# Performance work log

Measured on AMD Instinct MI355X. Metric: run time of the kernel, lower is better.

## Reference

```python
import jax, jax.numpy as jnp
import numpy as np
from jax import lax

B, C_IN, T = 256, 1, 1632
HID, CB_DIM, NUM_TOK, NUM_Q = 64, 512, 1024, 2


def conv_k2s2(x, W, b):
    # Conv1d(kernel=2, stride=2): x [B,Ci,T] -> [B,Co,T//2]; W [Co,Ci,2]
    Bx, Ci, Tx = x.shape
    xr = x.reshape(Bx, Ci, Tx // 2, 2)
    return jnp.einsum('bitk,oik->bot', xr, W) + b[None, :, None]


def convT_k2s2(x, W, b):
    # ConvTranspose1d(kernel=2, stride=2): x [B,Ci,T] -> [B,Co,2T]; W [Ci,Co,2] (torch layout)
    Bx, Ci, Tx = x.shape
    y = jnp.einsum('bit,iok->botk', x, W)  # [B,Co,T,2]
    Co = W.shape[1]
    return y.reshape(Bx, Co, 2 * Tx) + b[None, :, None]


def conv1x1(x, W, b):
    # W [Co,Ci]
    return jnp.einsum('bit,oi->bot', x, W) + b[None, :, None]


def residual_vq(x, codebooks):
    # x [B,t,D]; codebooks [NUM_Q, NUM_TOK, D]. Euclidean argmin + straight-through.
    residual = x
    quantized_out = jnp.zeros_like(x)
    all_idx, all_loss = [], []
    for q in range(codebooks.shape[0]):
        cb = codebooks[q]  # [N,D]
        # squared euclidean distance, single large GEMM
        d2 = (jnp.sum(residual ** 2, -1, keepdims=True)
              - 2.0 * jnp.einsum('btd,nd->btn', residual, cb)
              + jnp.sum(cb ** 2, -1))  # [B,t,N]
        idx = jnp.argmin(d2, axis=-1)  # [B,t]
        quant = cb[idx]  # gather [B,t,D]
        # commitment loss (codebook treated as fixed / EMA-updated)
        loss = jnp.mean((lax.stop_gradient(quant) - residual) ** 2)
        # straight-through estimator
        quant_st = residual + lax.stop_gradient(quant - residual)
        residual = residual - lax.stop_gradient(quant)
        quantized_out = quantized_out + quant_st
        all_idx.append(idx)
        all_loss.append(loss)
    return quantized_out, jnp.stack(all_idx, -1), jnp.stack(all_loss)


def setup_inputs() -> dict:
    key = jax.random.key(0)
    ks = jax.random.split(key, 16)
    s = 0.02
    return {
        'img': jax.random.normal(ks[0], (B, C_IN, T), jnp.float32),
        'W_e1': jax.random.normal(ks[1], (HID, C_IN, 2), jnp.float32) * s,
        'b_e1': jnp.zeros((HID,), jnp.float32),
        'W_e2': jax.random.normal(ks[2], (HID, HID, 2), jnp.float32) * s,
        'b_e2': jnp.zeros((HID,), jnp.float32),
        'W_e3': jax.random.normal(ks[3], (CB_DIM, HID), jnp.float32) * s,
        'b_e3': jnp.zeros((CB_DIM,), jnp.float32),
        'codebooks': jax.random.normal(ks[4], (NUM_Q, NUM_TOK, CB_DIM), jnp.float32),
        'Wt_d1': jax.random.normal(ks[5], (CB_DIM, HID, 2), jnp.float32) * s,
        'b_d1': jnp.zeros((HID,), jnp.float32),
        'Wt_d2': jax.random.normal(ks[6], (HID, HID, 2), jnp.float32) * s,
        'b_d2': jnp.zeros((HID,), jnp.float32),
        'W_d3': jax.random.normal(ks[7], (C_IN, HID), jnp.float32) * s,
        'b_d3': jnp.zeros((C_IN,), jnp.float32),
    }


def reference(img, W_e1, b_e1, W_e2, b_e2, W_e3, b_e3, codebooks,
              Wt_d1, b_d1, Wt_d2, b_d2, W_d3, b_d3):
    # encoder
    h = jax.nn.relu(conv_k2s2(img, W_e1, b_e1))
    h = jax.nn.relu(conv_k2s2(h, W_e2, b_e2))
    encoded = conv1x1(h, W_e3, b_e3)  # [B,512,408]
    # residual VQ over tokens
    x = jnp.transpose(encoded, (0, 2, 1))  # b c t -> b t c
    quantized, indices, commit_loss = residual_vq(x, codebooks)
    quantized = jnp.transpose(quantized, (0, 2, 1))  # b t c -> b c t
    # decoder
    d = jax.nn.relu(convT_k2s2(quantized, Wt_d1, b_d1))
    d = jax.nn.relu(convT_k2s2(d, Wt_d2, b_d2))
    out = conv1x1(d, W_d3, b_d3)  # [B,1,1632]
    recon_loss = jnp.mean((img - out) ** 2)
    return out, recon_loss, commit_loss, indices, quantized
```

## Files before the change

### kernel.cpp

```cpp
#include <hip/hip_runtime.h>

#define NB    256
#define TLEN  1632
#define HIDC  64
#define CBD   512
#define NTOK  1024
#define T2L   816
#define T4L   408
#define MTOK  (NB*T4L)
#define M2TOK (NB*T2L)
#define MOUT  (NB*TLEN)

#define DO_OUT    ((size_t)0)
#define DO_RECON  ((size_t)417792)
#define DO_IDX    ((size_t)417795)
#define DO_QUANT  ((size_t)626691)

typedef unsigned short u16;
typedef unsigned long long u64;
typedef __attribute__((ext_vector_type(8))) short short8;
typedef __attribute__((ext_vector_type(4))) float f32x4;
typedef __attribute__((ext_vector_type(8))) _Float16 half8;
typedef __attribute__((ext_vector_type(4))) _Float16 half4;

static constexpr size_t OFF_XR  = 0;
static constexpr size_t OFF_H1  = OFF_XR + (size_t)MTOK*512;
static constexpr size_t OFF_H2  = OFF_H1 + (size_t)NB*T2L*64;
static constexpr size_t OFF_BE2 = OFF_H2 + (size_t)NB*T4L*64;
static constexpr size_t OFF_BD1 = OFF_BE2 + 8192;
static constexpr size_t OFF_BD2 = OFF_BD1 + 65536;
static constexpr size_t OFF_BX1 = OFF_BD2 + 8192;
static constexpr size_t OFF_BX2 = OFF_BX1 + 128;
static constexpr size_t OFF_ZB  = OFF_BX2 + 128;
static constexpr size_t OFF_C2  = OFF_ZB + 128;
static constexpr size_t OFF_SLOT= OFF_C2 + 2048;
static constexpr size_t OFF_IDXI= OFF_SLOT + 1536;
static constexpr size_t OFF_KEYS= OFF_IDXI + (size_t)MTOK*2;
static constexpr size_t OFF_FC  = OFF_KEYS + (size_t)MTOK*4;
static constexpr size_t OFF_FLAG= OFF_FC + 4;
static constexpr size_t OFF_CBH = OFF_FLAG + (size_t)MTOK*2;
static constexpr size_t OFF_CBL = OFF_CBH + 524288;
static constexpr size_t OFF_P0  = OFF_CBL + 524288;
static constexpr size_t OFF_P1  = OFF_P0 + 131072;
static constexpr size_t OFF_PAIRS = OFF_P1 + 131072;

__device__ inline u64 shfl_xor_u64_w16(u64 v, int m) {
    unsigned lo = (unsigned)v, hi = (unsigned)(v >> 32);
    lo = __shfl_xor(lo, m, 16);
    hi = __shfl_xor(hi, m, 16);
    return (((u64)hi) << 32) | lo;
}
__device__ inline u64 packkey(float d, int n) {
    unsigned u = __float_as_uint(d);
    u = (u & 0x80000000u) ? ~u : (u | 0x80000000u);
    return (((u64)u) << 32) | (unsigned)n;
}
__device__ inline float unpackd(u64 k) {
    unsigned u = (unsigned)(k >> 32);
    u = (u & 0x80000000u) ? (u & 0x7fffffffu) : ~u;
    return __uint_as_float(u);
}
__device__ inline void merge2(u64& k1, u64& k2, u64 o1, u64 o2) {
    u64 n1 = (k1 < o1) ? k1 : o1;
    u64 hi = (k1 < o1) ? o1 : k1;
    u64 cand = (k1 <= o1) ? k2 : o2;
    u64 n2 = (hi < cand) ? hi : cand;
    k1 = n1; k2 = n2;
}
__device__ inline half4 cvt_h4(float4 v) {
    half4 h;
    h.x = (_Float16)v.x; h.y = (_Float16)v.y;
    h.z = (_Float16)v.z; h.w = (_Float16)v.w;
    return h;
}

__global__ void setup_kernel(const float* __restrict__ We2, const float* __restrict__ Wtd1,
                             const float* __restrict__ Wtd2, const float* __restrict__ bd1,
                             const float* __restrict__ bd2, const float* __restrict__ cbs,
                             float* __restrict__ Be2, float* __restrict__ Bd1,
                             float* __restrict__ Bd2, float* __restrict__ bx1, float* __restrict__ bx2,
                             u16* __restrict__ cbh, float* __restrict__ c2) {
    size_t t = (size_t)blockIdx.x * 256 + threadIdx.x;
    {
        float4 v = *(const float4*)(cbs + t * 4);
        *(half4*)&cbh[t * 4] = cvt_h4(v);
    }
    {
        int w = (int)(t >> 6);
        int lane = threadIdx.x & 63;
        if (w < 2048) {
            const float* r = cbs + (size_t)w * 512;
            float4 a = *(const float4*)(r + lane * 8);
            float4 b = *(const float4*)(r + lane * 8 + 4);
            float s = a.x*a.x + a.y*a.y + a.z*a.z + a.w*a.w + b.x*b.x + b.y*b.y + b.z*b.z + b.w*b.w;
            #pragma unroll
            for (int o = 32; o > 0; o >>= 1) s += __shfl_down(s, o, 64);
            if (lane == 0) c2[w] = s;
        }
    }
    size_t stride = (size_t)gridDim.x * 256;
    for (size_t x = t; x < 64 * 128; x += stride) {
        int c = (int)(x >> 7), k = (int)(x & 127);
        Be2[x] = We2[c * 128 + ((k & 63) << 1) + (k >> 6)];
    }
    for (size_t x = t; x < 128 * 512; x += stride) {
        int n = (int)(x >> 9), k = (int)(x & 511);
        Bd1[x] = Wtd1[k * 128 + n];
    }
    for (size_t x = t; x < 128 * 64; x += stride) {
        int n = (int)(x >> 6), k = (int)(x & 63);
        Bd2[x] = Wtd2[k * 128 + n];
    }
    for (size_t x = t; x < 128; x += stride) { bx1[x] = bd1[x >> 1]; bx2[x] = bd2[x >> 1]; }
}

__global__ void enc1_kernel(const float* __restrict__ img, const float* __restrict__ W,
                            const float* __restrict__ bias, float* __restrict__ h1) {
    int idx = blockIdx.x * 256 + threadIdx.x;
    int c = idx & 63;
    int t = (idx >> 6) % T2L;
    int b = idx / (64 * T2L);
    float v = W[c * 2] * img[(size_t)b * TLEN + 2 * t] +
              W[c * 2 + 1] * img[(size_t)b * TLEN + 2 * t + 1] + bias[c];
    h1[idx] = fmaxf(v, 0.f);
}

__global__ __launch_bounds__(256) void gemm_nt(const float* __restrict__ A, const float* __restrict__ Bw,
                        const float* __restrict__ bias, float* __restrict__ C,
                        int M, int N, int K, int amode, int relu) {
    __shared__ float As[32][132];
    __shared__ float Bs[32][68];
    int m0 = blockIdx.x * 128;
    int n0 = blockIdx.y * 64;
    int tid = threadIdx.x;
    int tx = tid & 15;
    int ty = tid >> 4;
    float acc[8][4];
    #pragma unroll
    for (int i = 0; i < 8; ++i)
        #pragma unroll
        for (int j = 0; j < 4; ++j) acc[i][j] = 0.f;

    for (int k0 = 0; k0 < K; k0 += 32) {
        #pragma unroll
        for (int i = 0; i < 4; ++i) {
            int idx = tid + i * 256;
            int row = idx >> 3;
            int kq = idx & 7;
            int m = m0 + row;
            size_t base;
            if (amode == 0) base = (size_t)m * K;
            else            base = (size_t)(((m / T4L) * T2L + 2 * (m % T4L)) * 64);
            float4 v = *(const float4*)(A + base + k0 + kq * 4);
            int kk = kq * 4;
            As[kk + 0][row] = v.x; As[kk + 1][row] = v.y;
            As[kk + 2][row] = v.z; As[kk + 3][row] = v.w;
        }
        #pragma unroll
        for (int i = 0; i < 2; ++i) {
            int idx = tid + i * 256;
            int row = idx >> 3;
            int kq = idx & 7;
            float4 v = *(const float4*)(Bw + (size_t)(n0 + row) * K + k0 + kq * 4);
            int kk = kq * 4;
            Bs[kk + 0][row] = v.x; Bs[kk + 1][row] = v.y;
            Bs[kk + 2][row] = v.z; Bs[kk + 3][row] = v.w;
        }
        __syncthreads();
        #pragma unroll
        for (int kk = 0; kk < 32; ++kk) {
            float a[8], bf[4];
            float4 a0 = *(const float4*)&As[kk][ty * 8];
            float4 a1 = *(const float4*)&As[kk][ty * 8 + 4];
            a[0]=a0.x; a[1]=a0.y; a[2]=a0.z; a[3]=a0.w;
            a[4]=a1.x; a[5]=a1.y; a[6]=a1.z; a[7]=a1.w;
            float4 b0 = *(const float4*)&Bs[kk][tx * 4];
            bf[0]=b0.x; bf[1]=b0.y; bf[2]=b0.z; bf[3]=b0.w;
            #pragma unroll
            for (int i = 0; i < 8; ++i)
                #pragma unroll
                for (int j = 0; j < 4; ++j) acc[i][j] += a[i] * bf[j];
        }
        __syncthreads();
    }
    #pragma unroll
    for (int i = 0; i < 8; ++i) {
        int m = m0 + ty * 8 + i;
        float4 v;
        v.x = acc[i][0] + bias[n0 + tx * 4 + 0];
        v.y = acc[i][1] + bias[n0 + tx * 4 + 1];
        v.z = acc[i][2] + bias[n0 + tx * 4 + 2];
        v.w = acc[i][3] + bias[n0 + tx * 4 + 3];
        if (relu) { v.x=fmaxf(v.x,0.f); v.y=fmaxf(v.y,0.f); v.z=fmaxf(v.z,0.f); v.w=fmaxf(v.w,0.f); }
        *(float4*)(C + (size_t)m * N + n0 + tx * 4) = v;
    }
}

template<int Q1>
__global__ __launch_bounds__(256, 2) void vq_f16_db(
    const float* __restrict__ Ap, const u16* __restrict__ cbh,
    const float* __restrict__ c2, const u64* __restrict__ prevkeys,
    const float* __restrict__ cb0, u64* __restrict__ pairs)
{
    __shared__ __align__(16) u16 As[2][128 * 40];
    __shared__ __align__(16) u16 Bh[2][256 * 40];
    int tid = threadIdx.x;
    int n0 = blockIdx.x * 256, m0 = blockIdx.y * 128;
    int lane = tid & 63, wid = tid >> 6;
    int lm = lane & 15, quad = lane >> 4;
    int wm = wid >> 1, wn = wid & 1;

    f32x4 acc[4][8];
    #pragma unroll
    for (int i = 0; i < 4; ++i)
        #pragma unroll
        for (int j = 0; j < 8; ++j) acc[i][j] = (f32x4){0.f, 0.f, 0.f, 0.f};

    int ar[4], acq[4], br[4], bcc[4];
    size_t coff[4];
    #pragma unroll
    for (int i = 0; i < 4; ++i) {
        int idx = tid + i * 256;
        ar[i] = idx >> 3; acq[i] = idx & 7;
        br[i] = idx >> 2; bcc[i] = idx & 3;
        if (Q1) {
            int i0 = (int)(prevkeys[m0 + ar[i]] & 0xFFFFFFFFull);
            coff[i] = (size_t)i0 * 512;
        }
    }

#define VQ_LOAD(K0, AV, CV, BV)                                                     \
    _Pragma("unroll")                                                               \
    for (int i = 0; i < 4; ++i) {                                                   \
        AV[i] = *(const float4*)(Ap + (size_t)(m0 + ar[i]) * 512 + (K0) + acq[i]*4);\
        if (Q1) CV[i] = *(const float4*)(cb0 + coff[i] + (K0) + acq[i]*4);          \
        BV[i] = *(const short8*)(cbh + (size_t)(n0 + br[i]) * 512 + (K0) + bcc[i]*8); \
    }

#define VQ_WRITE(BUF, AV, CV, BV)                                                   \
    _Pragma("unroll")                                                               \
    for (int i = 0; i < 4; ++i) {                                                   \
        float4 v = AV[i];                                                           \
        if (Q1) { v.x -= CV[i].x; v.y -= CV[i].y; v.z -= CV[i].z; v.w -= CV[i].w; } \
        *(half4*)&As[BUF][ar[i] * 40 + acq[i] * 4] = cvt_h4(v);                     \
        *(short8*)&Bh[BUF][br[i] * 40 + bcc[i] * 8] = BV[i];                        \
    }

#define VQ_COMPUTE(BUF) {                                                           \
        half8 ah[4];                                                                \
        _Pragma("unroll")                                                           \
        for (int mt = 0; mt < 4; ++mt)                                              \
            ah[mt] = *(const half8*)&As[BUF][(wm*64 + mt*16 + lm) * 40 + quad * 8]; \
        _Pragma("unroll")                                                           \
        for (int nt = 0; nt < 8; ++nt) {                                            \
            half8 bh = *(const half8*)&Bh[BUF][(wn*128 + nt*16 + lm) * 40 + quad*8];\
            _Pragma("unroll")                                                       \
            for (int mt = 0; mt < 4; ++mt)                                          \
                acc[mt][nt] = __builtin_amdgcn_mfma_f32_16x16x32_f16(ah[mt], bh, acc[mt][nt], 0, 0, 0); \
        }                                                                           \
    }

    float4 avA[4], cvA[4], avB[4], cvB[4];
    short8 bvA[4], bvB[4];
    (void)cvA; (void)cvB;

    VQ_LOAD(0, avA, cvA, bvA);
    VQ_WRITE(0, avA, cvA, bvA);
    VQ_LOAD(32, avB, cvB, bvB);
    __syncthreads();

    for (int tp = 0; tp < 8; ++tp) {
        {
            VQ_WRITE(1, avB, cvB, bvB);
            if (tp < 7) { int K0 = (2 * tp + 2) * 32; VQ_LOAD(K0, avA, cvA, bvA); }
            VQ_COMPUTE(0);
            __syncthreads();
        }
        {
            if (tp < 7) { VQ_WRITE(0, avA, cvA, bvA); }
            if (tp < 7) { int K0 = (2 * tp + 3) * 32; VQ_LOAD(K0, avB, cvB, bvB); }
            VQ_COMPUTE(1);
            __syncthreads();
        }
    }
#undef VQ_LOAD
#undef VQ_WRITE
#undef VQ_COMPUTE

    float c2v[8];
    #pragma unroll
    for (int nt = 0; nt < 8; ++nt) c2v[nt] = c2[n0 + wn * 128 + nt * 16 + lm];

    u64* scr = (u64*)&As[0][0];
    #pragma unroll
    for (int mt = 0; mt < 4; ++mt) {
        #pragma unroll
        for (int rg = 0; rg < 4; ++rg) {
            int tl = wm * 64 + mt * 16 + quad * 4 + rg;
            u64 k1 = ~0ull, k2 = ~0ull;
            #pragma unroll
            for (int nt = 0; nt < 8; ++nt) {
                float d = c2v[nt] - 2.0f * acc[mt][nt][rg];
                u64 k = packkey(d, n0 + wn * 128 + nt * 16 + lm);
                if (k < k1) { k2 = k1; k1 = k; } else if (k < k2) { k2 = k; }
            }
            #pragma unroll
            for (int s = 1; s < 16; s <<= 1) {
                u64 o1 = shfl_xor_u64_w16(k1, s);
                u64 o2 = shfl_xor_u64_w16(k2, s);
                merge2(k1, k2, o1, o2);
            }
            if (lm == 0) { scr[wn * 256 + tl * 2] = k1; scr[wn * 256 + tl * 2 + 1] = k2; }
        }
    }
    __syncthreads();
    if (tid < 128) {
        u64 a1 = scr[tid * 2], a2 = scr[tid * 2 + 1];
        merge2(a1, a2, scr[256 + tid * 2], scr[256 + tid * 2 + 1]);
        size_t base = (size_t)(m0 + tid) * 8 + blockIdx.x * 2;
        pairs[base] = a1; pairs[base + 1] = a2;
    }
}

__global__ void vq_reduce(const u64* __restrict__ pairs, u64* __restrict__ keybuf,
                          int* __restrict__ fc, int* __restrict__ flaglist, float tau) {
    int m = blockIdx.x * 256 + threadIdx.x;
    const u64* p = pairs + (size_t)m * 8;
    u64 k1 = ~0ull, k2 = ~0ull;
    #pragma unroll
    for (int i = 0; i < 8; ++i) {
        u64 k = p[i];
        if (k < k1) { k2 = k1; k1 = k; } else if (k < k2) { k2 = k; }
    }
    keybuf[m] = k1;
    if (unpackd(k2) - unpackd(k1) < tau) {
        int pos = atomicAdd(fc, 1);
        flaglist[pos] = m;
    }
}

__global__ void vq_rescue(const float* __restrict__ xr, const float* __restrict__ cb,
                          const float* __restrict__ c2, const float* __restrict__ cb0,
                          const u64* __restrict__ prevkeys,
                          const int* __restrict__ fc, const int* __restrict__ flaglist,
                          u64* __restrict__ keybuf) {
    __shared__ u64 red[4];
    int cnt = *fc;
    int lane = threadIdx.x & 63, wid = threadIdx.x >> 6;
    for (int f = blockIdx.x; f < cnt; f += gridDim.x) {
        int m = flaglist[f];
        float4 rv0 = *(const float4*)(xr + (size_t)m * 512 + lane * 8);
        float4 rv1 = *(const float4*)(xr + (size_t)m * 512 + lane * 8 + 4);
        if (cb0) {
            size_t co = (size_t)(prevkeys[m] & 0xFFFFFFFFull) * 512;
            float4 c0 = *(const float4*)(cb0 + co + lane * 8);
            float4 c1 = *(const float4*)(cb0 + co + lane * 8 + 4);
            rv0.x -= c0.x; rv0.y -= c0.y; rv0.z -= c0.z; rv0.w -= c0.w;
            rv1.x -= c1.x; rv1.y -= c1.y; rv1.z -= c1.z; rv1.w -= c1.w;
        }
        u64 best = ~0ull;
        for (int c = wid * 256; c < wid * 256 + 256; ++c) {
            const float* cp = cb + (size_t)c * 512 + lane * 8;
            float4 c0 = *(const float4*)cp;
            float4 c1 = *(const float4*)(cp + 4);
            float p = rv0.x*c0.x + rv0.y*c0.y + rv0.z*c0.z + rv0.w*c0.w
                    + rv1.x*c1.x + rv1.y*c1.y + rv1.z*c1.z + rv1.w*c1.w;
            #pragma unroll
            for (int s = 1; s < 64; s <<= 1) p += __shfl_xor(p, s, 64);
            u64 k = packkey(c2[c] - 2.0f * p, c);
            if (k < best) best = k;
        }
        if (lane == 0) red[wid] = best;
        __syncthreads();
        if (threadIdx.x == 0) {
            u64 b = red[0];
            if (red[1] < b) b = red[1];
            if (red[2] < b) b = red[2];
            if (red[3] < b) b = red[3];
            keybuf[m] = b;
        }
        __syncthreads();
    }
}

__global__ void commit_idx_kernel(const float* __restrict__ xr,
                                  const float* __restrict__ cb0f, const float* __restrict__ cb1f,
                                  const u64* __restrict__ keys0, const u64* __restrict__ keys1,
                                  float* __restrict__ idx_f, int* __restrict__ idx_i,
                                  float* __restrict__ slots) {
    int tid = threadIdx.x;
    int lane = tid & 63;
    int m = blockIdx.x * 4 + (tid >> 6);
    unsigned i0 = (unsigned)(keys0[m] & 0xFFFFFFFFull);
    unsigned i1 = (unsigned)(keys1[m] & 0xFFFFFFFFull);
    const float* x = xr + (size_t)m * 512 + lane * 8;
    const float* c0 = cb0f + (size_t)i0 * 512 + lane * 8;
    const float* c1 = cb1f + (size_t)i1 * 512 + lane * 8;
    float4 x0 = *(const float4*)x, x1 = *(const float4*)(x + 4);
    float4 a0 = *(const float4*)c0, a1 = *(const float4*)(c0 + 4);
    float4 b0 = *(const float4*)c1, b1 = *(const float4*)(c1 + 4);
    x0.x -= a0.x; x0.y -= a0.y; x0.z -= a0.z; x0.w -= a0.w;
    x1.x -= a1.x; x1.y -= a1.y; x1.z -= a1.z; x1.w -= a1.w;
    float s1 = x0.x*x0.x + x0.y*x0.y + x0.z*x0.z + x0.w*x0.w
             + x1.x*x1.x + x1.y*x1.y + x1.z*x1.z + x1.w*x1.w;
    x0.x -= b0.x; x0.y -= b0.y; x0.z -= b0.z; x0.w -= b0.w;
    x1.x -= b1.x; x1.y -= b1.y; x1.z -= b1.z; x1.w -= b1.w;
    float s2 = x0.x*x0.x + x0.y*x0.y + x0.z*x0.z + x0.w*x0.w
             + x1.x*x1.x + x1.y*x1.y + x1.z*x1.z + x1.w*x1.w;
    #pragma unroll
    for (int o = 32; o > 0; o >>= 1) { s1 += __shfl_down(s1, o, 64); s2 += __shfl_down(s2, o, 64); }
    if (lane == 0) {
        atomicAdd(&slots[512 + (m & 511)], s1);
        atomicAdd(&slots[1024 + (m & 511)], s2);
        idx_f[(size_t)m * 2]     = (float)i0;
        idx_f[(size_t)m * 2 + 1] = (float)i1;
        idx_i[m * 2] = (int)i0;
        idx_i[m * 2 + 1] = (int)i1;
    }
}

__global__ void quant_out_kernel(const float* __restrict__ cb0, const float* __restrict__ cb1,
                                 const int* __restrict__ idxi, float* __restrict__ out4) {
    __shared__ float buf[64][129];
    __shared__ int i0s[64], i1s[64];
    int b = blockIdx.x;
    int t0 = blockIdx.y * 64;
    int c0 = blockIdx.z * 128;
    int tid = threadIdx.x;
    if (tid < 64) {
        int t = t0 + tid;
        int i0 = 0, i1 = 0;
        if (t < T4L) { i0 = idxi[(b * T4L + t) * 2]; i1 = idxi[(b * T4L + t) * 2 + 1]; }
        i0s[tid] = i0; i1s[tid] = i1;
    }
    __syncthreads();
    int cl = tid & 127, th = tid >> 7;
    for (int t = th; t < 64; t += 2) {
        if (t0 + t < T4L)
            buf[t][cl] = cb0[(size_t)i0s[t] * 512 + c0 + cl] + cb1[(size_t)i1s[t] * 512 + c0 + cl];
    }
    __syncthreads();
    int lane = tid & 63, ch = tid >> 6;
    for (int cc = ch; cc < 128; cc += 4) {
        int t = t0 + lane;
        if (t < T4L) out4[((size_t)b * 512 + c0 + cc) * T4L + t] = buf[lane][cc];
    }
}

__global__ void d1_gather_kernel(const float* __restrict__ P0, const float* __restrict__ P1,
                                 const int* __restrict__ idxi, const float* __restrict__ bx1,
                                 float* __restrict__ d1) {
    int x = blockIdx.x * 256 + threadIdx.x;
    int n = x & 127;
    int m = x >> 7;
    int b = m / T4L, t = m % T4L;
    int i0 = idxi[m * 2], i1 = idxi[m * 2 + 1];
    float v = P0[i0 * 128 + n] + P1[i1 * 128 + n] + bx1[n];
    v = fmaxf(v, 0.f);
    d1[((size_t)(b * T2L + 2 * t + (n & 1))) * 64 + (n >> 1)] = v;
}

__global__ __launch_bounds__(256) void dec2_fused(
    const float* __restrict__ d1, const float* __restrict__ Bd2, const float* __restrict__ bx2,
    const float* __restrict__ W3, const float* __restrict__ b3, const float* __restrict__ img,
    float* __restrict__ out, float* __restrict__ slots)
{
    __shared__ float As[32][132];
    __shared__ float Bs[32][132];
    __shared__ float w3s[64];
    int m0 = blockIdx.x * 128;
    int tid = threadIdx.x;
    int tx = tid & 15;
    int ty = tid >> 4;
    if (tid < 64) w3s[tid] = W3[tid];
    float acc[8][8];
    #pragma unroll
    for (int i = 0; i < 8; ++i)
        #pragma unroll
        for (int j = 0; j < 8; ++j) acc[i][j] = 0.f;

    for (int k0 = 0; k0 < 64; k0 += 32) {
        #pragma unroll
        for (int i = 0; i < 4; ++i) {
            int idx = tid + i * 256;
            int row = idx >> 3;
            int kq = idx & 7;
            float4 v = *(const float4*)(d1 + (size_t)(m0 + row) * 64 + k0 + kq * 4);
            int kk = kq * 4;
            As[kk + 0][row] = v.x; As[kk + 1][row] = v.y;
            As[kk + 2][row] = v.z; As[kk + 3][row] = v.w;
        }
        #pragma unroll
        for (int i = 0; i < 4; ++i) {
            int idx = tid + i * 256;
            int row = idx >> 3;
            int kq = idx & 7;
            float4 v = *(const float4*)(Bd2 + (size_t)row * 64 + k0 + kq * 4);
            int kk = kq * 4;
            Bs[kk + 0][row] = v.x; Bs[kk + 1][row] = v.y;
            Bs[kk + 2][row] = v.z; Bs[kk + 3][row] = v.w;
        }
        __syncthreads();
        #pragma unroll
        for (int kk = 0; kk < 32; ++kk) {
            float a[8], bf[8];
            float4 a0 = *(const float4*)&As[kk][ty * 8];
            float4 a1 = *(const float4*)&As[kk][ty * 8 + 4];
            a[0]=a0.x; a[1]=a0.y; a[2]=a0.z; a[3]=a0.w;
            a[4]=a1.x; a[5]=a1.y; a[6]=a1.z; a[7]=a1.w;
            float4 b0 = *(const float4*)&Bs[kk][tx * 4];
            float4 b1 = *(const float4*)&Bs[kk][64 + tx * 4];
            bf[0]=b0.x; bf[1]=b0.y; bf[2]=b0.z; bf[3]=b0.w;
            bf[4]=b1.x; bf[5]=b1.y; bf[6]=b1.z; bf[7]=b1.w;
            #pragma unroll
            for (int i = 0; i < 8; ++i)
                #pragma unroll
                for (int j = 0; j < 8; ++j) acc[i][j] += a[i] * bf[j];
        }
        __syncthreads();
    }
    float bb3 = b3[0];
    float local = 0.f;
    #pragma unroll
    for (int i = 0; i < 8; ++i) {
        float s0 = 0.f, s1 = 0.f;
        #pragma unroll
        for (int j = 0; j < 4; ++j) {
            int n = tx * 4 + j;
            float v = fmaxf(acc[i][j] + bx2[n], 0.f);
            float w = w3s[n >> 1];
            if (j & 1) s1 += w * v; else s0 += w * v;
            int n2 = 64 + tx * 4 + j;
            float v2 = fmaxf(acc[i][j + 4] + bx2[n2], 0.f);
            float w2 = w3s[n2 >> 1];
            if (j & 1) s1 += w2 * v2; else s0 += w2 * v2;
        }
        #pragma unroll
        for (int o = 8; o > 0; o >>= 1) { s0 += __shfl_down(s0, o, 16); s1 += __shfl_down(s1, o, 16); }
        if (tx == 0) {
            int m = m0 + ty * 8 + i;
            int b = m / T2L, t2 = m % T2L;
            size_t o0 = (size_t)b * TLEN + 2 * t2;
            float v0 = s0 + bb3, v1 = s1 + bb3;
            out[o0] = v0; out[o0 + 1] = v1;
            float e0 = img[o0] - v0, e1 = img[o0 + 1] - v1;
            local += e0 * e0 + e1 * e1;
        }
    }
    if (tx == 0) atomicAdd(&slots[(blockIdx.x * 16 + ty) & 511], local);
}

__global__ void finalize_kernel(const float* __restrict__ slots, float* __restrict__ out_scalars) {
    __shared__ float red[256];
    int tid = threadIdx.x;
    for (int which = 0; which < 3; ++which) {
        float s = slots[which * 512 + tid] + slots[which * 512 + tid + 256];
        red[tid] = s; __syncthreads();
        for (int st = 128; st > 0; st >>= 1) { if (tid < st) red[tid] += red[tid + st]; __syncthreads(); }
        if (tid == 0) {
            float denom = (which == 0) ? (float)MOUT : (float)((size_t)MTOK * 512);
            out_scalars[which] = red[0] / denom;
        }
        __syncthreads();
    }
}

extern "C" void kernel_launch(void* const* d_in, const int* in_sizes, int n_in,
                              void* d_out, int out_size, void* d_ws, size_t ws_size,
                              hipStream_t stream) {
    const float* img  = (const float*)d_in[0];
    const float* We1  = (const float*)d_in[1];
    const float* be1  = (const float*)d_in[2];
    const float* We2  = (const float*)d_in[3];
    const float* be2  = (const float*)d_in[4];
    const float* We3  = (const float*)d_in[5];
    const float* be3  = (const float*)d_in[6];
    const float* cbs  = (const float*)d_in[7];
    const float* Wtd1 = (const float*)d_in[8];
    const float* bd1  = (const float*)d_in[9];
    const float* Wtd2 = (const float*)d_in[10];
    const float* bd2  = (const float*)d_in[11];
    const float* Wd3  = (const float*)d_in[12];
    const float* bd3  = (const float*)d_in[13];

    float* w = (float*)d_ws;
    float* xr   = w + OFF_XR;
    float* h1   = w + OFF_H1;
    float* h2   = w + OFF_H2;
    float* Be2  = w + OFF_BE2;
    float* Bd1  = w + OFF_BD1;
    float* Bd2  = w + OFF_BD2;
    float* bx1  = w + OFF_BX1;
    float* bx2  = w + OFF_BX2;
    float* zerob= w + OFF_ZB;
    float* c2   = w + OFF_C2;
    float* slots= w + OFF_SLOT;
    int*   idxi = (int*)(w + OFF_IDXI);
    u64*   keys = (u64*)(w + OFF_KEYS);
    int*   fc   = (int*)(w + OFF_FC);
    int*   flag = (int*)(w + OFF_FLAG);
    u16*   cbh  = (u16*)(w + OFF_CBH);
    float* P0   = w + OFF_P0;
    float* P1   = w + OFF_P1;
    u64*   pairs= (u64*)(w + OFF_PAIRS);

    float* outp = (float*)d_out;
    float* out0   = outp + DO_OUT;
    float* oscal  = outp + DO_RECON;
    float* idxf   = outp + DO_IDX;
    float* qout   = outp + DO_QUANT;

    hipMemsetAsync(slots, 0, 1536 * sizeof(float), stream);
    hipMemsetAsync(fc, 0, 2 * sizeof(int), stream);
    hipMemsetAsync(zerob, 0, 128 * sizeof(float), stream);

    setup_kernel<<<1024, 256, 0, stream>>>(We2, Wtd1, Wtd2, bd1, bd2, cbs,
                                           Be2, Bd1, Bd2, bx1, bx2, cbh, c2);

    const float* cb1p = cbs + (size_t)NTOK * CBD;

    gemm_nt<<<dim3(8, 2), 256, 0, stream>>>(cbs,  Bd1, zerob, P0, 1024, 128, 512, 0, 0);
    gemm_nt<<<dim3(8, 2), 256, 0, stream>>>(cb1p, Bd1, zerob, P1, 1024, 128, 512, 0, 0);

    enc1_kernel<<<(NB * T2L * HIDC) / 256, 256, 0, stream>>>(img, We1, be1, h1);
    gemm_nt<<<dim3(MTOK / 128, 1), 256, 0, stream>>>(h1, Be2, be2, h2, MTOK, 64, 128, 1, 1);
    gemm_nt<<<dim3(MTOK / 128, 8), 256, 0, stream>>>(h2, We3, be3, xr, MTOK, 512, 64, 0, 0);

    vq_f16_db<0><<<dim3(4, MTOK / 128), 256, 0, stream>>>(xr, cbh, c2, nullptr, nullptr, pairs);
    vq_reduce<<<MTOK / 256, 256, 0, stream>>>(pairs, keys, fc + 0, flag, 0.05f);
    vq_rescue<<<1024, 256, 0, stream>>>(xr, cbs, c2, nullptr, nullptr, fc + 0, flag, keys);
    vq_f16_db<1><<<dim3(4, MTOK / 128), 256, 0, stream>>>(xr, cbh + (size_t)NTOK * 512,
                                                          c2 + NTOK, keys, cbs, pairs);
    vq_reduce<<<MTOK / 256, 256, 0, stream>>>(pairs, keys + MTOK, fc + 1, flag + MTOK, 0.15f);
    vq_rescue<<<1024, 256, 0, stream>>>(xr, cb1p, c2 + NTOK, cbs, keys, fc + 1, flag + MTOK, keys + MTOK);

    commit_idx_kernel<<<MTOK / 4, 256, 0, stream>>>(xr, cbs, cb1p, keys, keys + MTOK, idxf, idxi, slots);

    quant_out_kernel<<<dim3(NB, 7, 4), 256, 0, stream>>>(cbs, cb1p, idxi, qout);

    d1_gather_kernel<<<(MTOK * 128) / 256, 256, 0, stream>>>(P0, P1, idxi, bx1, h1);
    dec2_fused<<<M2TOK / 128, 256, 0, stream>>>(h1, Bd2, bx2, Wd3, bd3, img, out0, slots);

    finalize_kernel<<<1, 256, 0, stream>>>(slots, oscal);
}
```

Before: 1.176 ms.

## Shrink VQ distance GEMM tile to 128x128 and subtract residual in fp16

The VQ distance GEMM tile drops from 128x256 to 128x128, which halves the accumulator registers and shared memory per block. Occupancy is raised to 3 blocks per CU, and the codebook dimension now uses 8 blocks instead of 4. The second-stage residual now subtracts the fp16 copy of the previous codeword instead of the fp32 one, which halves that gather traffic but adds extra rounding error before the argmin. Candidate pairs per token double to 16, and the pairs buffer now reuses the h2 scratch region, so each A tile is loaded twice as often.

```diff
diff --git a/kernel.cpp b/kernel.cpp
--- a/kernel.cpp
+++ b/kernel.cpp
@@ -42,7 +42,6 @@
 static constexpr size_t OFF_CBL = OFF_CBH + 524288;
 static constexpr size_t OFF_P0  = OFF_CBL + 524288;
 static constexpr size_t OFF_P1  = OFF_P0 + 131072;
-static constexpr size_t OFF_PAIRS = OFF_P1 + 131072;
 
 __device__ inline u64 shfl_xor_u64_w16(u64 v, int m) {
     unsigned lo = (unsigned)v, hi = (unsigned)(v >> 32);
@@ -71,6 +70,14 @@
     half4 h;
     h.x = (_Float16)v.x; h.y = (_Float16)v.y;
     h.z = (_Float16)v.z; h.w = (_Float16)v.w;
+    return h;
+}
+__device__ inline half8 cvt_h8(float4 v0, float4 v1) {
+    half8 h;
+    h[0] = (_Float16)v0.x; h[1] = (_Float16)v0.y;
+    h[2] = (_Float16)v0.z; h[3] = (_Float16)v0.w;
+    h[4] = (_Float16)v1.x; h[5] = (_Float16)v1.y;
+    h[6] = (_Float16)v1.z; h[7] = (_Float16)v1.w;
     return h;
 }
 
@@ -197,88 +204,89 @@
 }
 
 template<int Q1>
-__global__ __launch_bounds__(256, 2) void vq_f16_db(
+__global__ __launch_bounds__(256, 3) void vq_f16_db(
     const float* __restrict__ Ap, const u16* __restrict__ cbh,
     const float* __restrict__ c2, const u64* __restrict__ prevkeys,
-    const float* __restrict__ cb0, u64* __restrict__ pairs)
+    const u16* __restrict__ cb0h, u64* __restrict__ pairs)
 {
     __shared__ __align__(16) u16 As[2][128 * 40];
-    __shared__ __align__(16) u16 Bh[2][256 * 40];
+    __shared__ __align__(16) u16 Bs[2][128 * 40];
     int tid = threadIdx.x;
-    int n0 = blockIdx.x * 256, m0 = blockIdx.y * 128;
+    int n0 = blockIdx.x * 128, m0 = blockIdx.y * 128;
     int lane = tid & 63, wid = tid >> 6;
     int lm = lane & 15, quad = lane >> 4;
     int wm = wid >> 1, wn = wid & 1;
 
-    f32x4 acc[4][8];
+    f32x4 acc[4][4];
     #pragma unroll
     for (int i = 0; i < 4; ++i)
         #pragma unroll
-        for (int j = 0; j < 8; ++j) acc[i][j] = (f32x4){0.f, 0.f, 0.f, 0.f};
-
-    int ar[4], acq[4], br[4], bcc[4];
-    size_t coff[4];
-    #pragma unroll
-    for (int i = 0; i < 4; ++i) {
+        for (int j = 0; j < 4; ++j) acc[i][j] = (f32x4){0.f, 0.f, 0.f, 0.f};
+
+    int rw[2], cq[2];
+    size_t coff[2];
+    #pragma unroll
+    for (int i = 0; i < 2; ++i) {
         int idx = tid + i * 256;
-        ar[i] = idx >> 3; acq[i] = idx & 7;
-        br[i] = idx >> 2; bcc[i] = idx & 3;
+        rw[i] = idx >> 2; cq[i] = idx & 3;
         if (Q1) {
-            int i0 = (int)(prevkeys[m0 + ar[i]] & 0xFFFFFFFFull);
+            int i0 = (int)(prevkeys[m0 + rw[i]] & 0xFFFFFFFFull);
             coff[i] = (size_t)i0 * 512;
         }
     }
 
-#define VQ_LOAD(K0, AV, CV, BV)                                                     \
-    _Pragma("unroll")                                                               \
-    for (int i = 0; i < 4; ++i) {                                                   \
-        AV[i] = *(const float4*)(Ap + (size_t)(m0 + ar[i]) * 512 + (K0) + acq[i]*4);\
-        if (Q1) CV[i] = *(const float4*)(cb0 + coff[i] + (K0) + acq[i]*4);          \
-        BV[i] = *(const short8*)(cbh + (size_t)(n0 + br[i]) * 512 + (K0) + bcc[i]*8); \
-    }
-
-#define VQ_WRITE(BUF, AV, CV, BV)                                                   \
-    _Pragma("unroll")                                                               \
-    for (int i = 0; i < 4; ++i) {                                                   \
-        float4 v = AV[i];                                                           \
-        if (Q1) { v.x -= CV[i].x; v.y -= CV[i].y; v.z -= CV[i].z; v.w -= CV[i].w; } \
-        *(half4*)&As[BUF][ar[i] * 40 + acq[i] * 4] = cvt_h4(v);                     \
-        *(short8*)&Bh[BUF][br[i] * 40 + bcc[i] * 8] = BV[i];                        \
-    }
-
-#define VQ_COMPUTE(BUF) {                                                           \
-        half8 ah[4];                                                                \
-        _Pragma("unroll")                                                           \
-        for (int mt = 0; mt < 4; ++mt)                                              \
-            ah[mt] = *(const half8*)&As[BUF][(wm*64 + mt*16 + lm) * 40 + quad * 8]; \
-        _Pragma("unroll")                                                           \
-        for (int nt = 0; nt < 8; ++nt) {                                            \
-            half8 bh = *(const half8*)&Bh[BUF][(wn*128 + nt*16 + lm) * 40 + quad*8];\
-            _Pragma("unroll")                                                       \
-            for (int mt = 0; mt < 4; ++mt)                                          \
+#define VQ_LOAD(K0, AV0, AV1, CH, BV)                                                 \
+    _Pragma("unroll")                                                                 \
+    for (int i = 0; i < 2; ++i) {                                                     \
+        AV0[i] = *(const float4*)(Ap + (size_t)(m0 + rw[i]) * 512 + (K0) + cq[i]*8);  \
+        AV1[i] = *(const float4*)(Ap + (size_t)(m0 + rw[i]) * 512 + (K0) + cq[i]*8 + 4);\
+        if (Q1) CH[i] = *(const half8*)(cb0h + coff[i] + (K0) + cq[i]*8);             \
+        BV[i] = *(const short8*)(cbh + (size_t)(n0 + rw[i]) * 512 + (K0) + cq[i]*8);  \
+    }
+
+#define VQ_WRITE(BUF, AV0, AV1, CH, BV)                                               \
+    _Pragma("unroll")                                                                 \
+    for (int i = 0; i < 2; ++i) {                                                     \
+        half8 hv = cvt_h8(AV0[i], AV1[i]);                                            \
+        if (Q1) hv = hv - CH[i];                                                      \
+        *(half8*)&As[BUF][rw[i] * 40 + cq[i] * 8] = hv;                               \
+        *(short8*)&Bs[BUF][rw[i] * 40 + cq[i] * 8] = BV[i];                           \
+    }
+
+#define VQ_COMPUTE(BUF) {                                                             \
+        half8 ah[4];                                                                  \
+        _Pragma("unroll")                                                             \
+        for (int mt = 0; mt < 4; ++mt)                                                \
+            ah[mt] = *(const half8*)&As[BUF][(wm*64 + mt*16 + lm) * 40 + quad * 8];   \
+        _Pragma("unroll")                                                             \
+        for (int nt = 0; nt < 4; ++nt) {                                              \
+            half8 bh = *(const half8*)&Bs[BUF][(wn*64 + nt*16 + lm) * 40 + quad * 8]; \
+            _Pragma("unroll")                                                         \
+            for (int mt = 0; mt < 4; ++mt)                                            \
                 acc[mt][nt] = __builtin_amdgcn_mfma_f32_16x16x32_f16(ah[mt], bh, acc[mt][nt], 0, 0, 0); \
-        }                                                                           \
-    }
-
-    float4 avA[4], cvA[4], avB[4], cvB[4];
-    short8 bvA[4], bvB[4];
-    (void)cvA; (void)cvB;
-
-    VQ_LOAD(0, avA, cvA, bvA);
-    VQ_WRITE(0, avA, cvA, bvA);
-    VQ_LOAD(32, avB, cvB, bvB);
+        }                                                                             \
+    }
+
+    float4 a0A[2], a1A[2], a0B[2], a1B[2];
+    half8 chA[2], chB[2];
+    short8 bvA[2], bvB[2];
+    (void)chA; (void)chB;
+
+    VQ_LOAD(0, a0A, a1A, chA, bvA);
+    VQ_WRITE(0, a0A, a1A, chA, bvA);
+    VQ_LOAD(32, a0B, a1B, chB, bvB);
     __syncthreads();
 
     for (int tp = 0; tp < 8; ++tp) {
         {
-            VQ_WRITE(1, avB, cvB, bvB);
-            if (tp < 7) { int K0 = (2 * tp + 2) * 32; VQ_LOAD(K0, avA, cvA, bvA); }
+            VQ_WRITE(1, a0B, a1B, chB, bvB);
+            if (tp < 7) { int K0 = (2 * tp + 2) * 32; VQ_LOAD(K0, a0A, a1A, chA, bvA); }
             VQ_COMPUTE(0);
             __syncthreads();
         }
         {
-            if (tp < 7) { VQ_WRITE(0, avA, cvA, bvA); }
-            if (tp < 7) { int K0 = (2 * tp + 3) * 32; VQ_LOAD(K0, avB, cvB, bvB); }
+            if (tp < 7) { VQ_WRITE(0, a0A, a1A, chA, bvA); }
+            if (tp < 7) { int K0 = (2 * tp + 3) * 32; VQ_LOAD(K0, a0B, a1B, chB, bvB); }
             VQ_COMPUTE(1);
             __syncthreads();
         }
@@ -287,9 +295,9 @@
 #undef VQ_WRITE
 #undef VQ_COMPUTE
 
-    float c2v[8];
-    #pragma unroll
-    for (int nt = 0; nt < 8; ++nt) c2v[nt] = c2[n0 + wn * 128 + nt * 16 + lm];
+    float c2v[4];
+    #pragma unroll
+    for (int nt = 0; nt < 4; ++nt) c2v[nt] = c2[n0 + wn * 64 + nt * 16 + lm];
 
     u64* scr = (u64*)&As[0][0];
     #pragma unroll
@@ -299,9 +307,9 @@
             int tl = wm * 64 + mt * 16 + quad * 4 + rg;
             u64 k1 = ~0ull, k2 = ~0ull;
             #pragma unroll
-            for (int nt = 0; nt < 8; ++nt) {
+            for (int nt = 0; nt < 4; ++nt) {
                 float d = c2v[nt] - 2.0f * acc[mt][nt][rg];
-                u64 k = packkey(d, n0 + wn * 128 + nt * 16 + lm);
+                u64 k = packkey(d, n0 + wn * 64 + nt * 16 + lm);
                 if (k < k1) { k2 = k1; k1 = k; } else if (k < k2) { k2 = k; }
             }
             #pragma unroll
@@ -317,7 +325,7 @@
     if (tid < 128) {
         u64 a1 = scr[tid * 2], a2 = scr[tid * 2 + 1];
         merge2(a1, a2, scr[256 + tid * 2], scr[256 + tid * 2 + 1]);
-        size_t base = (size_t)(m0 + tid) * 8 + blockIdx.x * 2;
+        size_t base = (size_t)(m0 + tid) * 16 + blockIdx.x * 2;
         pairs[base] = a1; pairs[base + 1] = a2;
     }
 }
@@ -325,10 +333,10 @@
 __global__ void vq_reduce(const u64* __restrict__ pairs, u64* __restrict__ keybuf,
                           int* __restrict__ fc, int* __restrict__ flaglist, float tau) {
     int m = blockIdx.x * 256 + threadIdx.x;
-    const u64* p = pairs + (size_t)m * 8;
+    const u64* p = pairs + (size_t)m * 16;
     u64 k1 = ~0ull, k2 = ~0ull;
     #pragma unroll
-    for (int i = 0; i < 8; ++i) {
+    for (int i = 0; i < 16; ++i) {
         u64 k = p[i];
         if (k < k1) { k2 = k1; k1 = k; } else if (k < k2) { k2 = k; }
     }
@@ -602,7 +610,7 @@
     u16*   cbh  = (u16*)(w + OFF_CBH);
     float* P0   = w + OFF_P0;
     float* P1   = w + OFF_P1;
-    u64*   pairs= (u64*)(w + OFF_PAIRS);
+    u64*   pairs= (u64*)(w + OFF_H2);
 
     float* outp = (float*)d_out;
     float* out0   = outp + DO_OUT;
@@ -626,11 +634,11 @@
     gemm_nt<<<dim3(MTOK / 128, 1), 256, 0, stream>>>(h1, Be2, be2, h2, MTOK, 64, 128, 1, 1);
     gemm_nt<<<dim3(MTOK / 128, 8), 256, 0, stream>>>(h2, We3, be3, xr, MTOK, 512, 64, 0, 0);
 
-    vq_f16_db<0><<<dim3(4, MTOK / 128), 256, 0, stream>>>(xr, cbh, c2, nullptr, nullptr, pairs);
+    vq_f16_db<0><<<dim3(8, MTOK / 128), 256, 0, stream>>>(xr, cbh, c2, nullptr, nullptr, pairs);
     vq_reduce<<<MTOK / 256, 256, 0, stream>>>(pairs, keys, fc + 0, flag, 0.05f);
     vq_rescue<<<1024, 256, 0, stream>>>(xr, cbs, c2, nullptr, nullptr, fc + 0, flag, keys);
-    vq_f16_db<1><<<dim3(4, MTOK / 128), 256, 0, stream>>>(xr, cbh + (size_t)NTOK * 512,
-                                                          c2 + NTOK, keys, cbs, pairs);
+    vq_f16_db<1><<<dim3(8, MTOK / 128), 256, 0, stream>>>(xr, cbh + (size_t)NTOK * 512,
+                                                          c2 + NTOK, keys, cbh, pairs);
     vq_reduce<<<MTOK / 256, 256, 0, stream>>>(pairs, keys + MTOK, fc + 1, flag + MTOK, 0.15f);
     vq_rescue<<<1024, 256, 0, stream>>>(xr, cb1p, c2 + NTOK, cbs, keys, fc + 1, flag + MTOK, keys + MTOK);
 
```

Result: slower. 1.319 ms (+12.2%).
